# Performance work log

Hardware: AMD Instinct MI355X
Metric: run time of the kernel (lower is better)

Reference implementation:

```python
import jax, jax.numpy as jnp
import numpy as np

THRESHOLD = 0.7


def ternary_dequant(w, threshold=THRESHOLD):
    """Ternary quantize {-1,0,+1} with masked-mean alpha, return ternary*alpha."""
    abs_w = jnp.abs(w)
    delta = threshold * jnp.mean(abs_w)
    ternary = jnp.where(w > delta, 1.0, jnp.where(w < -delta, -1.0, 0.0)).astype(w.dtype)
    nz = ternary != 0
    cnt = jnp.sum(nz)
    # alpha = mean(|w| over nonzero ternary entries); fall back to mean(|w|) if all-zero
    masked_sum = jnp.sum(jnp.where(nz, abs_w, 0.0))
    alpha = jnp.where(cnt > 0, masked_sum / jnp.maximum(cnt, 1).astype(w.dtype), jnp.mean(abs_w))
    return ternary * alpha


def setup_inputs() -> dict:
    key = jax.random.key(0)
    kx, kw, kb = jax.random.split(key, 3)
    B, S, D_IN, D_OUT = 4, 2048, 4096, 4096
    x = jax.random.normal(kx, (B * S, D_IN), dtype=jnp.float32)
    # xavier-uniform-ish init for latent FP32 weights
    limit = np.sqrt(6.0 / (D_IN + D_OUT)).astype(np.float32)
    weight = jax.random.uniform(kw, (D_OUT, D_IN), dtype=jnp.float32, minval=-limit, maxval=limit)
    bias = jax.random.normal(kb, (D_OUT,), dtype=jnp.float32) * 0.02
    return {"x": x, "weight": weight, "bias": bias}


def reference(x, weight, bias):
    q_weight = ternary_dequant(weight)  # (out, in)
    return jnp.matmul(x, q_weight.T) + bias  # (tokens, out)
```

## Files before the change

### kernel.cpp

```cpp
#include <hip/hip_runtime.h>

#define M_DIM 8192
#define N_DIM 4096
#define K_DIM 4096

typedef __attribute__((ext_vector_type(8))) __bf16 bf16x8;
typedef __attribute__((ext_vector_type(4))) __bf16 bf16x4;
typedef __attribute__((ext_vector_type(4))) float floatx4;

__device__ __forceinline__ void async_copy16(const void* g, void* l) {
    __builtin_amdgcn_global_load_lds(
        (const __attribute__((address_space(1))) void*)g,
        (__attribute__((address_space(3))) void*)l,
        16, 0, 0);
}

__device__ __forceinline__ double wave_reduce_d(double v) {
    #pragma unroll
    for (int o = 32; o > 0; o >>= 1) v += __shfl_down(v, o, 64);
    return v;
}
__device__ __forceinline__ unsigned wave_reduce_u(unsigned v) {
    #pragma unroll
    for (int o = 32; o > 0; o >>= 1) v += __shfl_down(v, o, 64);
    return v;
}

__global__ __launch_bounds__(256) void k_pre(const float4* __restrict__ w4,
                                             double* __restrict__ part,
                                             const float4* __restrict__ x4,
                                             bf16x4* __restrict__ xb) {
    const int tid = threadIdx.x;
    if (blockIdx.x < 2048) {
        int idx = blockIdx.x * 256 + tid;
        double s = 0.0;
        #pragma unroll
        for (int it = 0; it < 8; ++it) {
            float4 v = w4[idx + it * (2048 * 256)];
            s += (double)fabsf(v.x) + (double)fabsf(v.y) +
                 (double)fabsf(v.z) + (double)fabsf(v.w);
        }
        s = wave_reduce_d(s);
        __shared__ double sm[4];
        if ((tid & 63) == 0) sm[tid >> 6] = s;
        __syncthreads();
        if (tid == 0) part[blockIdx.x] = sm[0] + sm[1] + sm[2] + sm[3];
    } else {
        int idx = (blockIdx.x - 2048) * 256 + tid;
        #pragma unroll
        for (int it = 0; it < 4; ++it) {
            int i = idx + it * (8192 * 256);
            float4 v = x4[i];
            bf16x4 o;
            o[0] = (__bf16)v.x; o[1] = (__bf16)v.y;
            o[2] = (__bf16)v.z; o[3] = (__bf16)v.w;
            xb[i] = o;
        }
    }
}

__global__ __launch_bounds__(256) void k_quant(const float4* __restrict__ w4,
                                               bf16x4* __restrict__ tern,
                                               const double* __restrict__ part,
                                               double* __restrict__ scal,
                                               double* __restrict__ pm,
                                               unsigned* __restrict__ pc) {
    const int tid = threadIdx.x;
    double s = 0.0;
    #pragma unroll
    for (int i = 0; i < 8; ++i) s += part[tid + i * 256];
    s = wave_reduce_d(s);
    __shared__ double sm[4];
    if ((tid & 63) == 0) sm[tid >> 6] = s;
    __syncthreads();
    const double mean = (sm[0] + sm[1] + sm[2] + sm[3]) * (1.0 / 16777216.0);
    const double delta = 0.7 * mean;
    if (blockIdx.x == 0 && tid == 0) scal[0] = mean;

    int idx = blockIdx.x * 256 + tid;
    double msum = 0.0;
    unsigned cnt = 0;
    #pragma unroll
    for (int it = 0; it < 8; ++it) {
        int i = idx + it * (2048 * 256);
        float4 v = w4[i];
        float e[4] = {v.x, v.y, v.z, v.w};
        bf16x4 o;
        #pragma unroll
        for (int c = 0; c < 4; ++c) {
            float wv = e[c];
            float t = ((double)wv > delta) ? 1.0f
                    : (((double)wv < -delta) ? -1.0f : 0.0f);
            if (t != 0.0f) { msum += (double)fabsf(wv); cnt++; }
            o[c] = (__bf16)t;
        }
        tern[i] = o;
    }
    msum = wave_reduce_d(msum);
    cnt  = wave_reduce_u(cnt);
    __shared__ double smd[4];
    __shared__ unsigned smu[4];
    if ((tid & 63) == 0) { smd[tid >> 6] = msum; smu[tid >> 6] = cnt; }
    __syncthreads();
    if (tid == 0) {
        pm[blockIdx.x] = smd[0] + smd[1] + smd[2] + smd[3];
        pc[blockIdx.x] = smu[0] + smu[1] + smu[2] + smu[3];
    }
}

__global__ __launch_bounds__(256) void ternary_gemm(
    const __bf16* __restrict__ A,
    const __bf16* __restrict__ B,
    const float*  __restrict__ bias,
    const double* __restrict__ scal,
    const double* __restrict__ pm,
    const unsigned* __restrict__ pc,
    float* __restrict__ C)
{
    __shared__ __attribute__((aligned(128))) __bf16 As[128 * 32];
    __shared__ __attribute__((aligned(128))) __bf16 Bs[128 * 32];
    __shared__ double smd[4];
    __shared__ unsigned smu[4];

    const int tid  = threadIdx.x;
    const int wave = tid >> 6;
    const int lane = tid & 63;
    const int quad = lane >> 4;
    const int l16  = lane & 15;
    const int wr = wave >> 1;
    const int wc = wave & 1;

    const int br = blockIdx.y;
    const int bc = blockIdx.x;

    const int srow = lane >> 2;
    const int scol = ((lane & 3) ^ ((srow >> 1) & 3)) * 8;
    const int c0 = wave * 2;

    const __bf16* gA0 = A + (size_t)(br * 128 + c0 * 16 + srow) * K_DIM + scol;
    const __bf16* gA1 = gA0 + 16 * K_DIM;
    const __bf16* gB0 = B + (size_t)(bc * 128 + c0 * 16 + srow) * K_DIM + scol;
    const __bf16* gB1 = gB0 + 16 * K_DIM;
    __bf16* lA0 = &As[c0 * 512];
    __bf16* lA1 = &As[(c0 + 1) * 512];
    __bf16* lB0 = &Bs[c0 * 512];
    __bf16* lB1 = &Bs[(c0 + 1) * 512];

    floatx4 acc[4][4] = {};

    const int swz = (quad ^ ((l16 >> 1) & 3)) * 8;
    const int a_off = (wr * 64 + l16) * 32 + swz;
    const int b_off = (wc * 64 + l16) * 32 + swz;

    for (int k0 = 0; k0 < K_DIM; k0 += 32) {
        async_copy16(gA0, lA0);
        async_copy16(gA1, lA1);
        async_copy16(gB0, lB0);
        async_copy16(gB1, lB1);
        gA0 += 32; gA1 += 32; gB0 += 32; gB1 += 32;
        __syncthreads();

        bf16x8 af[4], bfr[4];
        #pragma unroll
        for (int i = 0; i < 4; ++i)
            af[i] = *(const bf16x8*)&As[a_off + i * 512];
        #pragma unroll
        for (int j = 0; j < 4; ++j)
            bfr[j] = *(const bf16x8*)&Bs[b_off + j * 512];

        #pragma unroll
        for (int i = 0; i < 4; ++i)
            #pragma unroll
            for (int j = 0; j < 4; ++j)
                acc[i][j] = __builtin_amdgcn_mfma_f32_16x16x32_bf16(
                    af[i], bfr[j], acc[i][j], 0, 0, 0);
        __syncthreads();
    }

    double s = 0.0; unsigned c = 0;
    #pragma unroll
    for (int i = 0; i < 8; ++i) { s += pm[tid + i * 256]; c += pc[tid + i * 256]; }
    s = wave_reduce_d(s);
    c = wave_reduce_u(c);
    if ((tid & 63) == 0) { smd[tid >> 6] = s; smu[tid >> 6] = c; }
    __syncthreads();
    const double ms = smd[0] + smd[1] + smd[2] + smd[3];
    const unsigned ct = smu[0] + smu[1] + smu[2] + smu[3];
    const float alpha = (float)(ct > 0 ? ms / (double)ct : scal[0]);

    float bv[4];
    #pragma unroll
    for (int j = 0; j < 4; ++j)
        bv[j] = bias[bc * 128 + wc * 64 + j * 16 + l16];

    #pragma unroll
    for (int i = 0; i < 4; ++i) {
        const int row0 = br * 128 + wr * 64 + i * 16 + quad * 4;
        #pragma unroll
        for (int j = 0; j < 4; ++j) {
            const int col = bc * 128 + wc * 64 + j * 16 + l16;
            #pragma unroll
            for (int r = 0; r < 4; ++r)
                C[(size_t)(row0 + r) * N_DIM + col] = acc[i][j][r] * alpha + bv[j];
        }
    }
}

extern "C" void kernel_launch(void* const* d_in, const int* in_sizes, int n_in,
                              void* d_out, int out_size, void* d_ws, size_t ws_size,
                              hipStream_t stream) {
    const float* x    = (const float*)d_in[0];
    const float* w    = (const float*)d_in[1];
    const float* bias = (const float*)d_in[2];
    float* out = (float*)d_out;

    char* ws = (char*)d_ws;
    double*   d_scal = (double*)ws;
    double*   part   = (double*)(ws + 64);
    double*   pm     = (double*)(ws + 16448);
    unsigned* pc     = (unsigned*)(ws + 32832);
    __bf16*   xb     = (__bf16*)(ws + 65536);
    __bf16*   tern   = (__bf16*)(ws + 65536 + (size_t)M_DIM * K_DIM * 2);

    k_pre<<<10240, 256, 0, stream>>>((const float4*)w, part, (const float4*)x, (bf16x4*)xb);
    k_quant<<<2048, 256, 0, stream>>>((const float4*)w, (bf16x4*)tern, part, d_scal, pm, pc);

    dim3 grid(N_DIM / 128, M_DIM / 128);
    ternary_gemm<<<grid, 256, 0, stream>>>(xb, tern, bias, d_scal, pm, pc, out);
}
```

Before: 578.6 us.

## Enlarge GEMM block tile to 256x128 with 8x4 MFMA tiles per wave

Doubles the M extent of each GEMM workgroup tile, so every wave computes a 128x64 sub-tile with 32 accumulators and loads 8 A fragments per k-step. The aim is more MFMA work per LDS load and barrier, and less re-fetching of B from global memory. In exchange register pressure rises sharply (acc doubles to 128 floats). Launch bounds now ask for 2 blocks per CU, which could cause spills. The grid is halved, leaving fewer workgroups to fill the CUs.

```diff
diff --git a/kernel.cpp b/kernel.cpp
--- a/kernel.cpp
+++ b/kernel.cpp
@@ -108,7 +108,7 @@
     }
 }
 
-__global__ __launch_bounds__(256) void ternary_gemm(
+__global__ __launch_bounds__(256, 2) void ternary_gemm(
     const __bf16* __restrict__ A,
     const __bf16* __restrict__ B,
     const float*  __restrict__ bias,
@@ -117,7 +117,7 @@
     const unsigned* __restrict__ pc,
     float* __restrict__ C)
 {
-    __shared__ __attribute__((aligned(128))) __bf16 As[128 * 32];
+    __shared__ __attribute__((aligned(128))) __bf16 As[256 * 32];
     __shared__ __attribute__((aligned(128))) __bf16 Bs[128 * 32];
     __shared__ double smd[4];
     __shared__ unsigned smu[4];
@@ -135,41 +135,47 @@
 
     const int srow = lane >> 2;
     const int scol = ((lane & 3) ^ ((srow >> 1) & 3)) * 8;
-    const int c0 = wave * 2;
-
-    const __bf16* gA0 = A + (size_t)(br * 128 + c0 * 16 + srow) * K_DIM + scol;
-    const __bf16* gA1 = gA0 + 16 * K_DIM;
-    const __bf16* gB0 = B + (size_t)(bc * 128 + c0 * 16 + srow) * K_DIM + scol;
-    const __bf16* gB1 = gB0 + 16 * K_DIM;
-    __bf16* lA0 = &As[c0 * 512];
-    __bf16* lA1 = &As[(c0 + 1) * 512];
-    __bf16* lB0 = &Bs[c0 * 512];
-    __bf16* lB1 = &Bs[(c0 + 1) * 512];
-
-    floatx4 acc[4][4] = {};
+
+    const __bf16* gA[4];
+    const __bf16* gB[2];
+    __bf16* lA[4];
+    __bf16* lB[2];
+    #pragma unroll
+    for (int t = 0; t < 4; ++t) {
+        const int c = wave * 4 + t;
+        gA[t] = A + (size_t)(br * 256 + c * 16 + srow) * K_DIM + scol;
+        lA[t] = &As[c * 512];
+    }
+    #pragma unroll
+    for (int t = 0; t < 2; ++t) {
+        const int c = wave * 2 + t;
+        gB[t] = B + (size_t)(bc * 128 + c * 16 + srow) * K_DIM + scol;
+        lB[t] = &Bs[c * 512];
+    }
+
+    floatx4 acc[8][4] = {};
 
     const int swz = (quad ^ ((l16 >> 1) & 3)) * 8;
-    const int a_off = (wr * 64 + l16) * 32 + swz;
+    const int a_off = (wr * 128 + l16) * 32 + swz;
     const int b_off = (wc * 64 + l16) * 32 + swz;
 
     for (int k0 = 0; k0 < K_DIM; k0 += 32) {
-        async_copy16(gA0, lA0);
-        async_copy16(gA1, lA1);
-        async_copy16(gB0, lB0);
-        async_copy16(gB1, lB1);
-        gA0 += 32; gA1 += 32; gB0 += 32; gB1 += 32;
+        #pragma unroll
+        for (int t = 0; t < 4; ++t) { async_copy16(gA[t], lA[t]); gA[t] += 32; }
+        #pragma unroll
+        for (int t = 0; t < 2; ++t) { async_copy16(gB[t], lB[t]); gB[t] += 32; }
         __syncthreads();
 
-        bf16x8 af[4], bfr[4];
-        #pragma unroll
-        for (int i = 0; i < 4; ++i)
+        bf16x8 af[8], bfr[4];
+        #pragma unroll
+        for (int i = 0; i < 8; ++i)
             af[i] = *(const bf16x8*)&As[a_off + i * 512];
         #pragma unroll
         for (int j = 0; j < 4; ++j)
             bfr[j] = *(const bf16x8*)&Bs[b_off + j * 512];
 
         #pragma unroll
-        for (int i = 0; i < 4; ++i)
+        for (int i = 0; i < 8; ++i)
             #pragma unroll
             for (int j = 0; j < 4; ++j)
                 acc[i][j] = __builtin_amdgcn_mfma_f32_16x16x32_bf16(
@@ -194,8 +200,8 @@
         bv[j] = bias[bc * 128 + wc * 64 + j * 16 + l16];
 
     #pragma unroll
-    for (int i = 0; i < 4; ++i) {
-        const int row0 = br * 128 + wr * 64 + i * 16 + quad * 4;
+    for (int i = 0; i < 8; ++i) {
+        const int row0 = br * 256 + wr * 128 + i * 16 + quad * 4;
         #pragma unroll
         for (int j = 0; j < 4; ++j) {
             const int col = bc * 128 + wc * 64 + j * 16 + l16;
@@ -225,6 +231,6 @@
     k_pre<<<10240, 256, 0, stream>>>((const float4*)w, part, (const float4*)x, (bf16x4*)xb);
     k_quant<<<2048, 256, 0, stream>>>((const float4*)w, (bf16x4*)tern, part, d_scal, pm, pc);
 
-    dim3 grid(N_DIM / 128, M_DIM / 128);
+    dim3 grid(N_DIM / 128, M_DIM / 256);
     ternary_gemm<<<grid, 256, 0, stream>>>(xb, tern, bias, d_scal, pm, pc, out);
 }
```

After: 554.7 us. 1.04x faster.
